# Kernel tuning notes

Measured on AMD Instinct MI355X. Metric: run time of the kernel, lower is better.

## Reference

```python
import jax, jax.numpy as jnp
import numpy as np

N, CIN, T, HF, WF = 1, 64, 8, 96, 96
C = 256
H, W = HF // 4, WF // 4
K = 27  # 3 dilations (1,3,5) x 3x3 kernel taps

# kernel-tap offsets, ordered: dilation-major, then row-major 3x3 (matches cat order)
_OFFS = np.array([(oy * d, ox * d) for d in (1, 3, 5) for oy in (-1, 0, 1) for ox in (-1, 0, 1)], dtype=np.float32)


def setup_inputs() -> dict:
    key = jax.random.key(0)
    ks = jax.random.split(key, 6)
    return {
        "input": jax.random.normal(ks[0], (N, CIN, T, HF, WF), jnp.float32),
        "flow": 2.0 * jax.random.normal(ks[1], (N, 2, T, H, W), jnp.float32),
        "w_node": 0.02 * jax.random.normal(ks[2], (C, CIN, 4, 4), jnp.float32),  # Conv3d(64,256,(1,4,4)) with unit time-kernel squeezed
        "b_node": jnp.zeros((C,), jnp.float32),
        "w_up": 0.02 * jax.random.normal(ks[3], (C, 64, 4, 4), jnp.float32),  # ConvTranspose3d(256,64,(1,4,4)) weight [in,out,kh,kw]
        "b_up": jnp.zeros((64,), jnp.float32),
        "w_out": 0.05 * jax.random.normal(ks[4], (64, 64), jnp.float32),  # 1x1x1 Conv3d(64,64)
        "b_out": jnp.zeros((64,), jnp.float32),
        "B": T,
    }


def _deform_sample(node, flow):
    # Deformable neighbor sampling for all 3 dilations at once.
    # node [N,C,T,H,W], flow [N,2,T,H,W] (y,x offsets) -> neighbour [N,C,T,H,W,K]
    n, c, t, h, w = node.shape
    off = jnp.asarray(_OFFS)  # [K,2]
    yy = jnp.arange(h, dtype=node.dtype)[:, None]   # [H,1]
    xx = jnp.arange(w, dtype=node.dtype)[None, :]   # [1,W]
    # sampling positions [N,T,K,H,W]
    py = (yy + off[:, 0][:, None, None]) + flow[:, 0][:, :, None]
    px = (xx + off[:, 1][:, None, None]) + flow[:, 1][:, :, None]
    y0 = jnp.floor(py)
    x0 = jnp.floor(px)
    ty = py - y0
    tx = px - x0
    y0 = y0.astype(jnp.int32)
    x0 = x0.astype(jnp.int32)
    nf = node.transpose(0, 2, 1, 3, 4).reshape(n, t, c, h * w)  # [N,T,C,HW]

    def gather(yi, xi):
        valid = ((yi >= 0) & (yi < h) & (xi >= 0) & (xi < w)).astype(node.dtype)
        idx = jnp.clip(yi, 0, h - 1) * w + jnp.clip(xi, 0, w - 1)  # [N,T,K,H,W]
        idx = jnp.broadcast_to(idx.reshape(n, t, 1, K * h * w), (n, t, c, K * h * w))
        v = jnp.take_along_axis(nf, idx, axis=-1).reshape(n, t, c, K, h, w)
        return v * valid[:, :, None]  # zero-pad outside

    samp = (gather(y0, x0) * ((1 - ty) * (1 - tx))[:, :, None]
            + gather(y0, x0 + 1) * ((1 - ty) * tx)[:, :, None]
            + gather(y0 + 1, x0) * (ty * (1 - tx))[:, :, None]
            + gather(y0 + 1, x0 + 1) * (ty * tx)[:, :, None])  # [N,T,C,K,H,W]
    return samp.transpose(0, 2, 1, 4, 5, 3)  # [N,C,T,H,W,K]


def reference(input, flow, w_node, b_node, w_up, b_up, w_out, b_out, B):
    n, cin, t, hf, wf = input.shape
    h, w = hf // 4, wf // 4
    # layer_node: kernel==stride (1,4,4) conv == non-overlapping 4x4 patch projection
    xr = input.reshape(n, cin, t, h, 4, w, 4)
    node = jnp.einsum('ncthawb,ocab->nothw', xr, w_node) + b_node[None, :, None, None, None]  # [N,C,T,H,W]
    c = node.shape[1]

    neighbour = _deform_sample(node, flow)  # [N,C,T,H,W,27] == cat(dcn1,dcn2,dcn3)

    nhw = n * h * w
    node_b = node.transpose(0, 3, 4, 2, 1).reshape(nhw, t, c)                      # [NHW,B,C]
    nb_a = neighbour.transpose(0, 3, 4, 1, 2, 5).reshape(nhw, c, t * K)            # [NHW,C,B*27]
    A = node_b @ nb_a                                                              # [NHW,B,B*27]
    nb_b = neighbour.transpose(0, 3, 4, 2, 5, 1).reshape(nhw, t * K, c)            # [NHW,B*27,C]
    out = (1.0 / 216.0) * (A @ nb_b)                                               # [NHW,B,C]
    out = out.reshape(n, h, w, t, c).transpose(0, 4, 3, 1, 2)                      # [N,C,T,H,W]

    # layer_out: ConvTranspose (k==stride, pad 0) == per-pixel 4x4 block expansion, then 1x1x1 conv
    up = jnp.einsum('ncthw,coab->nothawb', out, w_up).reshape(n, 64, t, 4 * h, 4 * w)
    up = up + b_up[None, :, None, None, None]
    return jnp.einsum('ncthw,oc->nothw', up, w_out) + b_out[None, :, None, None, None]
```

## Files before the change

kernel.cpp:

```cpp
#include <hip/hip_runtime.h>


typedef unsigned short ushort_t;
typedef ushort_t ushort8 __attribute__((ext_vector_type(8)));
typedef __bf16 bf16x8 __attribute__((ext_vector_type(8)));
typedef __bf16 bf16x2 __attribute__((ext_vector_type(2)));
typedef float f32x4 __attribute__((ext_vector_type(4)));
typedef unsigned int uint4v __attribute__((ext_vector_type(4)));

#define NSTR 264
#define TSTR 34
#define ASTR 40

__device__ __forceinline__ ushort_t f2bf(float f) {
    __bf16 h = (__bf16)f;
    return __builtin_bit_cast(ushort_t, h);
}
__device__ __forceinline__ float blo(unsigned u) { return __uint_as_float(u << 16); }
__device__ __forceinline__ float bhi(unsigned u) { return __uint_as_float(u & 0xffff0000u); }
__device__ __forceinline__ unsigned pk2(float a, float b) {
    bf16x2 v = { (__bf16)a, (__bf16)b };
    return __builtin_bit_cast(unsigned, v);
}
__device__ __forceinline__ unsigned pk2h(__bf16 a, __bf16 b) {
    bf16x2 v = { a, b };
    return __builtin_bit_cast(unsigned, v);
}
__device__ __forceinline__ void gld_lds16(const void* g, void* l) {
    __builtin_amdgcn_global_load_lds(
        (const __attribute__((address_space(1))) unsigned*)g,
        (__attribute__((address_space(3))) unsigned*)l, 16, 0, 0);
}

__global__ __launch_bounds__(256) void k_prep(
    const float* __restrict__ w_node, const float* __restrict__ w_up,
    const float* __restrict__ w_out, const float* __restrict__ b_up,
    const float* __restrict__ b_out,
    ushort_t* __restrict__ w_node_perm, ushort_t* __restrict__ Wf_perm,
    float* __restrict__ bias_tot)
{
    __shared__ float wout_s[4096];
    int tid = threadIdx.x;
    for (int i = tid; i < 4096; i += 256) wout_s[i] = w_out[i];
    __syncthreads();
    int gid = blockIdx.x * 256 + tid;
    #pragma unroll
    for (int r = 0; r < 4; ++r) {
        int e = gid + r * 65536;
        {
            int k = e & 1023, n = e >> 10;
            w_node_perm[(((k >> 3) << 8) + n) * 8 + (k & 7)] = f2bf(w_node[n * 1024 + k]);
        }
        {
            int n = e & 1023, k = e >> 10;
            int o = n >> 4, ab = n & 15;
            const float* wo = wout_s + o * 64;
            const float* wu = w_up + (k << 10) + ab;
            float s = 0.f;
            #pragma unroll 8
            for (int c = 0; c < 64; ++c) s += wo[c] * wu[c << 4];
            Wf_perm[(((k >> 3) << 10) + n) * 8 + (k & 7)] = f2bf(s);
        }
    }
    if (blockIdx.x == 0 && tid < 64) {
        float s = b_out[tid];
        const float* wo = wout_s + tid * 64;
        #pragma unroll 8
        for (int c = 0; c < 64; ++c) s += wo[c] * b_up[c];
        bias_tot[tid] = s;
    }
}

template<int FINAL>
__global__ __launch_bounds__(256) void k_gemm(
    const float* __restrict__ input, const ushort_t* __restrict__ a_bf,
    const ushort_t* __restrict__ w_perm, const float* __restrict__ bias,
    ushort_t* __restrict__ node_bf, float* __restrict__ dout)
{
    constexpr int KS = FINAL ? 4 : 16;
    constexpr int N  = FINAL ? 1024 : 256;
    __shared__ __align__(16) ushort_t A_lds[2][2048];
    __shared__ __align__(16) ushort_t B_lds[2][8192];
    int tid  = threadIdx.x;
    int lane = tid & 63, wid = tid >> 6;
    int g = lane >> 4, r16 = lane & 15;
    int m0 = blockIdx.x * 32, n0 = blockIdx.y * 128;

    const float*   inpA = nullptr;
    const ushort_t* finA = nullptr;
    int ldsA_slot;
    if constexpr (!FINAL) {
        int mA = tid & 31, kcA = tid >> 5;
        int m = m0 + mA;
        int t = m / 576, hw = m % 576, hh = hw / 24, ww = hw % 24;
        inpA = input + (size_t)(kcA >> 1) * 73728 + t * 9216 + hh * 384 + ww * 4 + (kcA & 1) * 192;
        ldsA_slot = (kcA * 32 + mA) * 8;
    } else {
        int m = m0 + (tid >> 3), q = tid & 7;
        finA = a_bf + m * 256 + ((q ^ (m & 7)) * 8);
        ldsA_slot = tid * 8;
    }

    f32x4 acc[2][2];
    #pragma unroll
    for (int i = 0; i < 2; ++i)
        #pragma unroll
        for (int j = 0; j < 2; ++j) acc[i][j] = (f32x4){0.f, 0.f, 0.f, 0.f};

    float4 fa, fb;
    #pragma unroll
    for (int r = 0; r < 4; ++r) {
        int s = r * 256 + tid;
        gld_lds16(w_perm + (size_t)(((s >> 7) * N + n0 + (s & 127)) * 8), &B_lds[0][s * 8]);
    }
    if constexpr (FINAL) {
        gld_lds16(finA, &A_lds[0][ldsA_slot]);
    } else {
        fa = *(const float4*)(inpA);
        fb = *(const float4*)(inpA + 96);
        uint4v p;
        p.x = pk2(fa.x, fa.y); p.y = pk2(fa.z, fa.w);
        p.z = pk2(fb.x, fb.y); p.w = pk2(fb.z, fb.w);
        *(uint4v*)&A_lds[0][ldsA_slot] = p;
    }
    __syncthreads();

    for (int kb = 0; kb < KS; ++kb) {
        int cur = kb & 1, nxt = cur ^ 1;
        bool more = (kb + 1 < KS);
        if (more) {
            #pragma unroll
            for (int r = 0; r < 4; ++r) {
                int s = r * 256 + tid;
                gld_lds16(w_perm + (size_t)((((kb + 1) * 8 + (s >> 7)) * N + n0 + (s & 127)) * 8),
                          &B_lds[nxt][s * 8]);
            }
            if constexpr (FINAL) {
                gld_lds16(finA + (kb + 1) * 64, &A_lds[nxt][ldsA_slot]);
            } else {
                fa = *(const float4*)(inpA + (size_t)(kb + 1) * 294912);
                fb = *(const float4*)(inpA + (size_t)(kb + 1) * 294912 + 96);
            }
        }
        bf16x8 af[2][2], bfr[2][2];
        #pragma unroll
        for (int mi = 0; mi < 2; ++mi)
            #pragma unroll
            for (int ks = 0; ks < 2; ++ks) {
                int idx;
                if constexpr (!FINAL) idx = ((ks * 4 + g) * 32 + mi * 16 + r16) * 8;
                else                  idx = (mi * 16 + r16) * 64 + (((ks * 4 + g) ^ (r16 & 7)) * 8);
                af[mi][ks] = __builtin_bit_cast(bf16x8, *(const ushort8*)&A_lds[cur][idx]);
            }
        #pragma unroll
        for (int ni = 0; ni < 2; ++ni)
            #pragma unroll
            for (int ks = 0; ks < 2; ++ks) {
                int idx = ((ks * 4 + g) * 128 + wid * 32 + ni * 16 + r16) * 8;
                bfr[ni][ks] = __builtin_bit_cast(bf16x8, *(const ushort8*)&B_lds[cur][idx]);
            }
        #pragma unroll
        for (int mi = 0; mi < 2; ++mi)
            #pragma unroll
            for (int ni = 0; ni < 2; ++ni)
                #pragma unroll
                for (int ks = 0; ks < 2; ++ks)
                    acc[mi][ni] = __builtin_amdgcn_mfma_f32_16x16x32_bf16(
                        af[mi][ks], bfr[ni][ks], acc[mi][ni], 0, 0, 0);
        if constexpr (!FINAL) {
            if (more) {
                uint4v p;
                p.x = pk2(fa.x, fa.y); p.y = pk2(fa.z, fa.w);
                p.z = pk2(fb.x, fb.y); p.w = pk2(fb.z, fb.w);
                *(uint4v*)&A_lds[nxt][ldsA_slot] = p;
            }
        }
        __syncthreads();
    }

    if constexpr (!FINAL) {
        #pragma unroll
        for (int ni = 0; ni < 2; ++ni) {
            int n = n0 + wid * 32 + ni * 16 + r16;
            float bv = bias[n];
            #pragma unroll
            for (int mi = 0; mi < 2; ++mi)
                #pragma unroll
                for (int rr = 0; rr < 4; ++rr) {
                    int m = m0 + mi * 16 + 4 * g + rr;
                    node_bf[(size_t)m * 256 + n] = f2bf(acc[mi][ni][rr] + bv);
                }
        }
    } else {
        #pragma unroll
        for (int ni = 0; ni < 2; ++ni) {
            int n = n0 + wid * 32 + ni * 16 + r16;
            int o = n >> 4, aa = (n >> 2) & 3, bb = n & 3;
            float bv = bias[o];
            #pragma unroll
            for (int mi = 0; mi < 2; ++mi)
                #pragma unroll
                for (int rr = 0; rr < 4; ++rr) {
                    int m = m0 + mi * 16 + 4 * g + rr;
                    int t = m / 576, hw = m % 576, hh = hw / 24, ww = hw % 24;
                    dout[((size_t)(o * 8 + t) * 96 + hh * 4 + aa) * 96 + ww * 4 + bb]
                        = acc[mi][ni][rr] + bv;
                }
        }
    }
}

__global__ __launch_bounds__(256) void k_attn(
    const ushort_t* __restrict__ node_bf, const float* __restrict__ flow,
    ushort_t* __restrict__ out_bf)
{
    __shared__ __align__(16) int      bases[224 * 4];
    __shared__ __align__(16) float    wts[224 * 4];
    __shared__ __align__(16) ushort_t neigh[32 * NSTR];
    __shared__ __align__(16) ushort_t neighT[256 * TSTR];
    __shared__ __align__(16) ushort_t A_s[16 * ASTR];

    int tid  = threadIdx.x;
    int pos  = blockIdx.x;
    int h    = pos / 24, w = pos % 24;
    int lane = tid & 63, wid = tid >> 6;
    int g    = lane >> 4, r16 = lane & 15;

    if (tid < 224) {
        int j = tid;
        float w00 = 0, w01 = 0, w10 = 0, w11 = 0;
        int b00 = 0, b01 = 0, b10 = 0, b11 = 0;
        if (j < 216) {
            int tt = j / 27, kk = j - tt * 27;
            int d  = 2 * (kk / 9) + 1;
            int oy = (kk / 3) % 3 - 1, ox = kk % 3 - 1;
            float fy = flow[tt * 576 + pos];
            float fx = flow[4608 + tt * 576 + pos];
            float py = (float)(h + oy * d) + fy;
            float px = (float)(w + ox * d) + fx;
            float fy0 = floorf(py), fx0 = floorf(px);
            int y0 = (int)fy0, x0 = (int)fx0;
            float ty = py - fy0, tx = px - fx0;
            int y0c = min(max(y0, 0), 23), y1c = min(max(y0 + 1, 0), 23);
            int x0c = min(max(x0, 0), 23), x1c = min(max(x0 + 1, 0), 23);
            float vy0 = (y0 >= 0 && y0 < 24) ? 1.f : 0.f;
            float vy1 = (y0 >= -1 && y0 < 23) ? 1.f : 0.f;
            float vx0 = (x0 >= 0 && x0 < 24) ? 1.f : 0.f;
            float vx1 = (x0 >= -1 && x0 < 23) ? 1.f : 0.f;
            w00 = (1.f - ty) * (1.f - tx) * vy0 * vx0;
            w01 = (1.f - ty) * tx * vy0 * vx1;
            w10 = ty * (1.f - tx) * vy1 * vx0;
            w11 = ty * tx * vy1 * vx1;
            int base_t = tt * 576 * 256;
            b00 = base_t + (y0c * 24 + x0c) * 256;
            b01 = base_t + (y0c * 24 + x1c) * 256;
            b10 = base_t + (y1c * 24 + x0c) * 256;
            b11 = base_t + (y1c * 24 + x1c) * 256;
        }
        bases[j * 4 + 0] = b00; bases[j * 4 + 1] = b01;
        bases[j * 4 + 2] = b10; bases[j * 4 + 3] = b11;
        wts[j * 4 + 0] = w00; wts[j * 4 + 1] = w01;
        wts[j * 4 + 2] = w10; wts[j * 4 + 3] = w11;
    }
    for (int i = tid; i < 320; i += 256) ((unsigned*)A_s)[i] = 0;

    bf16x8 nbf[8];
    if (wid < 2) {
        int t = r16;
        const ushort_t* src = node_bf + ((size_t)(t & 7) * 576 + pos) * 256 + g * 8;
        ushort8 uz = {};
        #pragma unroll
        for (int s = 0; s < 8; ++s) {
            ushort8 uu = *(const ushort8*)(src + s * 32);
            nbf[s] = __builtin_bit_cast(bf16x8, (t < 8) ? uu : uz);
        }
    }

    f32x4 oacc[4];
    #pragma unroll
    for (int i = 0; i < 4; ++i) oacc[i] = (f32x4){0.f, 0.f, 0.f, 0.f};

    __syncthreads();

    const int jp = tid >> 4;
    const int cb = tid & 15;

    uint4v rg[2][8];
    #define PREFETCH(TILE) {                                                   \
        int jA_ = (TILE) * 32 + jp * 2;                                        \
        int4 bsA_ = *(const int4*)&bases[jA_ * 4];                             \
        int4 bsB_ = *(const int4*)&bases[jA_ * 4 + 4];                         \
        _Pragma("unroll")                                                      \
        for (int q_ = 0; q_ < 2; ++q_) {                                       \
            int c0_ = cb * 16 + q_ * 8;                                        \
            rg[q_][0] = *(const uint4v*)(node_bf + bsA_.x + c0_);              \
            rg[q_][1] = *(const uint4v*)(node_bf + bsA_.y + c0_);              \
            rg[q_][2] = *(const uint4v*)(node_bf + bsA_.z + c0_);              \
            rg[q_][3] = *(const uint4v*)(node_bf + bsA_.w + c0_);              \
            rg[q_][4] = *(const uint4v*)(node_bf + bsB_.x + c0_);              \
            rg[q_][5] = *(const uint4v*)(node_bf + bsB_.y + c0_);              \
            rg[q_][6] = *(const uint4v*)(node_bf + bsB_.z + c0_);              \
            rg[q_][7] = *(const uint4v*)(node_bf + bsB_.w + c0_);              \
        } }

    PREFETCH(0);

    for (int tile = 0; tile < 7; ++tile) {
        {
            int jA = tile * 32 + jp * 2;
            int jl = jp * 2;
            float4 wA = *(const float4*)&wts[jA * 4];
            float4 wB = *(const float4*)&wts[jA * 4 + 4];
            #pragma unroll
            for (int q = 0; q < 2; ++q) {
                int c0 = cb * 16 + q * 8;
                uint4v outA, outB;
                #pragma unroll
                for (int p = 0; p < 4; ++p) {
                    unsigned a0 = rg[q][0][p], a1 = rg[q][1][p], a2 = rg[q][2][p], a3 = rg[q][3][p];
                    unsigned b0 = rg[q][4][p], b1 = rg[q][5][p], b2 = rg[q][6][p], b3 = rg[q][7][p];
                    float aL = wA.x * blo(a0) + wA.y * blo(a1) + wA.z * blo(a2) + wA.w * blo(a3);
                    float aH = wA.x * bhi(a0) + wA.y * bhi(a1) + wA.z * bhi(a2) + wA.w * bhi(a3);
                    float bL = wB.x * blo(b0) + wB.y * blo(b1) + wB.z * blo(b2) + wB.w * blo(b3);
                    float bH = wB.x * bhi(b0) + wB.y * bhi(b1) + wB.z * bhi(b2) + wB.w * bhi(b3);
                    __bf16 cAL = (__bf16)aL, cAH = (__bf16)aH;
                    __bf16 cBL = (__bf16)bL, cBH = (__bf16)bH;
                    outA[p] = pk2h(cAL, cAH);
                    outB[p] = pk2h(cBL, cBH);
                    *(unsigned*)(neighT + (c0 + 2 * p) * TSTR + jl)     = pk2h(cAL, cBL);
                    *(unsigned*)(neighT + (c0 + 2 * p + 1) * TSTR + jl) = pk2h(cAH, cBH);
                }
                *(uint4v*)(neigh + jl * NSTR + c0)       = outA;
                *(uint4v*)(neigh + (jl + 1) * NSTR + c0) = outB;
            }
        }
        if (tile < 6) PREFETCH(tile + 1);
        __syncthreads();

        if (wid < 2) {
            f32x4 aacc = {0.f, 0.f, 0.f, 0.f};
            int jbase = wid * 16;
            #pragma unroll
            for (int s = 0; s < 8; ++s) {
                const ushort_t* bp = neigh + (jbase + r16) * NSTR + s * 32 + g * 8;
                bf16x8 bfrag = __builtin_bit_cast(bf16x8, *(const ushort8*)bp);
                aacc = __builtin_amdgcn_mfma_f32_16x16x32_bf16(nbf[s], bfrag, aacc, 0, 0, 0);
            }
            if (g < 2) {
                #pragma unroll
                for (int rr = 0; rr < 4; ++rr)
                    A_s[(4 * g + rr) * ASTR + jbase + r16] = f2bf(aacc[rr] * (1.f / 216.f));
            }
        }
        __syncthreads();

        {
            bf16x8 afrag = __builtin_bit_cast(bf16x8, *(const ushort8*)(A_s + r16 * ASTR + g * 8));
            #pragma unroll
            for (int i = 0; i < 4; ++i) {
                const ushort_t* tp = neighT + (wid * 64 + i * 16 + r16) * TSTR + g * 8;
                uint4v uv;
                uv.x = *(const unsigned*)(tp);
                uv.y = *(const unsigned*)(tp + 2);
                uv.z = *(const unsigned*)(tp + 4);
                uv.w = *(const unsigned*)(tp + 6);
                bf16x8 bfrag = __builtin_bit_cast(bf16x8, uv);
                oacc[i] = __builtin_amdgcn_mfma_f32_16x16x32_bf16(afrag, bfrag, oacc[i], 0, 0, 0);
            }
        }
        __syncthreads();
    }
    #undef PREFETCH

    if (g < 2) {
        #pragma unroll
        for (int i = 0; i < 4; ++i) {
            int c = wid * 64 + i * 16 + r16;
            #pragma unroll
            for (int rr = 0; rr < 4; ++rr) {
                int t = 4 * g + rr;
                out_bf[((size_t)t * 576 + pos) * 256 + c] = f2bf(oacc[i][rr]);
            }
        }
    }
}

extern "C" void kernel_launch(void* const* d_in, const int* in_sizes, int n_in,
                              void* d_out, int out_size, void* d_ws, size_t ws_size,
                              hipStream_t stream) {
    (void)in_sizes; (void)n_in; (void)out_size; (void)ws_size;
    const float* input  = (const float*)d_in[0];
    const float* flow   = (const float*)d_in[1];
    const float* w_node = (const float*)d_in[2];
    const float* b_node = (const float*)d_in[3];
    const float* w_up   = (const float*)d_in[4];
    const float* b_up   = (const float*)d_in[5];
    const float* w_out  = (const float*)d_in[6];
    const float* b_out  = (const float*)d_in[7];
    float* dout = (float*)d_out;

    char* wsb = (char*)d_ws;
    ushort_t* node_bf = (ushort_t*)wsb;
    ushort_t* out_bf  = (ushort_t*)(wsb + 2359296);
    ushort_t* w_np    = (ushort_t*)(wsb + 4718592);
    ushort_t* wf_p    = (ushort_t*)(wsb + 5242880);
    float*    bias_t  = (float*)(wsb + 5767168);

    k_prep<<<256, 256, 0, stream>>>(w_node, w_up, w_out, b_up, b_out, w_np, wf_p, bias_t);
    k_gemm<0><<<dim3(144, 2), 256, 0, stream>>>(input, nullptr, w_np, b_node, node_bf, nullptr);
    k_attn<<<576, 256, 0, stream>>>(node_bf, flow, out_bf);
    k_gemm<1><<<dim3(144, 8), 256, 0, stream>>>(nullptr, out_bf, wf_p, bias_t, nullptr, dout);
}
```

Baseline: 74.84 us.

## Double-buffer attention neighbor tiles and narrow node GEMM N-tile

The attention kernel now double-buffers the neighbour tiles in dynamic shared memory, so the gather/combine for the next tile runs alongside the MFMA work on the current tile. This removes one barrier per tile. The first GEMM's N tile shrinks from 128 to 64, which doubles its grid to raise occupancy on a small problem. The cost is more LDS per attention block (about 77KB), which may lower occupancy, and each GEMM block does less reuse of the A tile.

```diff
diff --git a/kernel.cpp b/kernel.cpp
--- a/kernel.cpp
+++ b/kernel.cpp
@@ -11,6 +11,15 @@
 #define NSTR 264
 #define TSTR 34
 #define ASTR 40
+
+#define OFF_NH0   0
+#define OFF_NH1   16896
+#define OFF_NT0   33792
+#define OFF_NT1   51200
+#define OFF_AS    68608
+#define OFF_BASES 69888
+#define OFF_WTS   73472
+#define ATTN_LDS  77056
 
 __device__ __forceinline__ ushort_t f2bf(float f) {
     __bf16 h = (__bf16)f;
@@ -79,12 +88,15 @@
 {
     constexpr int KS = FINAL ? 4 : 16;
     constexpr int N  = FINAL ? 1024 : 256;
+    constexpr int BN = FINAL ? 128 : 64;
+    constexpr int NI = FINAL ? 2 : 1;
+    constexpr int RB = BN / 32;
     __shared__ __align__(16) ushort_t A_lds[2][2048];
-    __shared__ __align__(16) ushort_t B_lds[2][8192];
+    __shared__ __align__(16) ushort_t B_lds[2][BN * 64];
     int tid  = threadIdx.x;
     int lane = tid & 63, wid = tid >> 6;
     int g = lane >> 4, r16 = lane & 15;
-    int m0 = blockIdx.x * 32, n0 = blockIdx.y * 128;
+    int m0 = blockIdx.x * 32, n0 = blockIdx.y * BN;
 
     const float*   inpA = nullptr;
     const ushort_t* finA = nullptr;
@@ -101,17 +113,18 @@
         ldsA_slot = tid * 8;
     }
 
-    f32x4 acc[2][2];
+    f32x4 acc[2][NI];
     #pragma unroll
     for (int i = 0; i < 2; ++i)
         #pragma unroll
-        for (int j = 0; j < 2; ++j) acc[i][j] = (f32x4){0.f, 0.f, 0.f, 0.f};
+        for (int j = 0; j < NI; ++j) acc[i][j] = (f32x4){0.f, 0.f, 0.f, 0.f};
 
     float4 fa, fb;
     #pragma unroll
-    for (int r = 0; r < 4; ++r) {
+    for (int r = 0; r < RB; ++r) {
         int s = r * 256 + tid;
-        gld_lds16(w_perm + (size_t)(((s >> 7) * N + n0 + (s & 127)) * 8), &B_lds[0][s * 8]);
+        int kc = s / BN, n = s % BN;
+        gld_lds16(w_perm + (size_t)((kc * N + n0 + n) * 8), &B_lds[0][s * 8]);
     }
     if constexpr (FINAL) {
         gld_lds16(finA, &A_lds[0][ldsA_slot]);
@@ -130,9 +143,10 @@
         bool more = (kb + 1 < KS);
         if (more) {
             #pragma unroll
-            for (int r = 0; r < 4; ++r) {
+            for (int r = 0; r < RB; ++r) {
                 int s = r * 256 + tid;
-                gld_lds16(w_perm + (size_t)((((kb + 1) * 8 + (s >> 7)) * N + n0 + (s & 127)) * 8),
+                int kc = s / BN, n = s % BN;
+                gld_lds16(w_perm + (size_t)((((kb + 1) * 8 + kc) * N + n0 + n) * 8),
                           &B_lds[nxt][s * 8]);
             }
             if constexpr (FINAL) {
@@ -142,7 +156,7 @@
                 fb = *(const float4*)(inpA + (size_t)(kb + 1) * 294912 + 96);
             }
         }
-        bf16x8 af[2][2], bfr[2][2];
+        bf16x8 af[2][2], bfr[NI][2];
         #pragma unroll
         for (int mi = 0; mi < 2; ++mi)
             #pragma unroll
@@ -153,16 +167,16 @@
                 af[mi][ks] = __builtin_bit_cast(bf16x8, *(const ushort8*)&A_lds[cur][idx]);
             }
         #pragma unroll
-        for (int ni = 0; ni < 2; ++ni)
+        for (int ni = 0; ni < NI; ++ni)
             #pragma unroll
             for (int ks = 0; ks < 2; ++ks) {
-                int idx = ((ks * 4 + g) * 128 + wid * 32 + ni * 16 + r16) * 8;
+                int idx = ((ks * 4 + g) * BN + wid * (BN / 4) + ni * 16 + r16) * 8;
                 bfr[ni][ks] = __builtin_bit_cast(bf16x8, *(const ushort8*)&B_lds[cur][idx]);
             }
         #pragma unroll
         for (int mi = 0; mi < 2; ++mi)
             #pragma unroll
-            for (int ni = 0; ni < 2; ++ni)
+            for (int ni = 0; ni < NI; ++ni)
                 #pragma unroll
                 for (int ks = 0; ks < 2; ++ks)
                     acc[mi][ni] = __builtin_amdgcn_mfma_f32_16x16x32_bf16(
@@ -179,21 +193,18 @@
     }
 
     if constexpr (!FINAL) {
-        #pragma unroll
-        for (int ni = 0; ni < 2; ++ni) {
-            int n = n0 + wid * 32 + ni * 16 + r16;
-            float bv = bias[n];
-            #pragma unroll
-            for (int mi = 0; mi < 2; ++mi)
-                #pragma unroll
-                for (int rr = 0; rr < 4; ++rr) {
-                    int m = m0 + mi * 16 + 4 * g + rr;
-                    node_bf[(size_t)m * 256 + n] = f2bf(acc[mi][ni][rr] + bv);
-                }
-        }
+        int n = n0 + wid * 16 + r16;
+        float bv = bias[n];
+        #pragma unroll
+        for (int mi = 0; mi < 2; ++mi)
+            #pragma unroll
+            for (int rr = 0; rr < 4; ++rr) {
+                int m = m0 + mi * 16 + 4 * g + rr;
+                node_bf[(size_t)m * 256 + n] = f2bf(acc[mi][0][rr] + bv);
+            }
     } else {
         #pragma unroll
-        for (int ni = 0; ni < 2; ++ni) {
+        for (int ni = 0; ni < NI; ++ni) {
             int n = n0 + wid * 32 + ni * 16 + r16;
             int o = n >> 4, aa = (n >> 2) & 3, bb = n & 3;
             float bv = bias[o];
@@ -214,11 +225,10 @@
     const ushort_t* __restrict__ node_bf, const float* __restrict__ flow,
     ushort_t* __restrict__ out_bf)
 {
-    __shared__ __align__(16) int      bases[224 * 4];
-    __shared__ __align__(16) float    wts[224 * 4];
-    __shared__ __align__(16) ushort_t neigh[32 * NSTR];
-    __shared__ __align__(16) ushort_t neighT[256 * TSTR];
-    __shared__ __align__(16) ushort_t A_s[16 * ASTR];
+    extern __shared__ char smem[];
+    ushort_t* A_s   = (ushort_t*)(smem + OFF_AS);
+    int*      bases = (int*)(smem + OFF_BASES);
+    float*    wts   = (float*)(smem + OFF_WTS);
 
     int tid  = threadIdx.x;
     int pos  = blockIdx.x;
@@ -284,65 +294,70 @@
 
     const int jp = tid >> 4;
     const int cb = tid & 15;
-
     uint4v rg[2][8];
-    #define PREFETCH(TILE) {                                                   \
-        int jA_ = (TILE) * 32 + jp * 2;                                        \
-        int4 bsA_ = *(const int4*)&bases[jA_ * 4];                             \
-        int4 bsB_ = *(const int4*)&bases[jA_ * 4 + 4];                         \
-        _Pragma("unroll")                                                      \
-        for (int q_ = 0; q_ < 2; ++q_) {                                       \
-            int c0_ = cb * 16 + q_ * 8;                                        \
-            rg[q_][0] = *(const uint4v*)(node_bf + bsA_.x + c0_);              \
-            rg[q_][1] = *(const uint4v*)(node_bf + bsA_.y + c0_);              \
-            rg[q_][2] = *(const uint4v*)(node_bf + bsA_.z + c0_);              \
-            rg[q_][3] = *(const uint4v*)(node_bf + bsA_.w + c0_);              \
-            rg[q_][4] = *(const uint4v*)(node_bf + bsB_.x + c0_);              \
-            rg[q_][5] = *(const uint4v*)(node_bf + bsB_.y + c0_);              \
-            rg[q_][6] = *(const uint4v*)(node_bf + bsB_.z + c0_);              \
-            rg[q_][7] = *(const uint4v*)(node_bf + bsB_.w + c0_);              \
-        } }
-
-    PREFETCH(0);
-
-    for (int tile = 0; tile < 7; ++tile) {
-        {
-            int jA = tile * 32 + jp * 2;
-            int jl = jp * 2;
-            float4 wA = *(const float4*)&wts[jA * 4];
-            float4 wB = *(const float4*)&wts[jA * 4 + 4];
-            #pragma unroll
-            for (int q = 0; q < 2; ++q) {
-                int c0 = cb * 16 + q * 8;
-                uint4v outA, outB;
-                #pragma unroll
-                for (int p = 0; p < 4; ++p) {
-                    unsigned a0 = rg[q][0][p], a1 = rg[q][1][p], a2 = rg[q][2][p], a3 = rg[q][3][p];
-                    unsigned b0 = rg[q][4][p], b1 = rg[q][5][p], b2 = rg[q][6][p], b3 = rg[q][7][p];
-                    float aL = wA.x * blo(a0) + wA.y * blo(a1) + wA.z * blo(a2) + wA.w * blo(a3);
-                    float aH = wA.x * bhi(a0) + wA.y * bhi(a1) + wA.z * bhi(a2) + wA.w * bhi(a3);
-                    float bL = wB.x * blo(b0) + wB.y * blo(b1) + wB.z * blo(b2) + wB.w * blo(b3);
-                    float bH = wB.x * bhi(b0) + wB.y * bhi(b1) + wB.z * bhi(b2) + wB.w * bhi(b3);
-                    __bf16 cAL = (__bf16)aL, cAH = (__bf16)aH;
-                    __bf16 cBL = (__bf16)bL, cBH = (__bf16)bH;
-                    outA[p] = pk2h(cAL, cAH);
-                    outB[p] = pk2h(cBL, cBH);
-                    *(unsigned*)(neighT + (c0 + 2 * p) * TSTR + jl)     = pk2h(cAL, cBL);
-                    *(unsigned*)(neighT + (c0 + 2 * p + 1) * TSTR + jl) = pk2h(cAH, cBH);
-                }
-                *(uint4v*)(neigh + jl * NSTR + c0)       = outA;
-                *(uint4v*)(neigh + (jl + 1) * NSTR + c0) = outB;
-            }
-        }
-        if (tile < 6) PREFETCH(tile + 1);
-        __syncthreads();
+
+    auto prefetch = [&](int TILE) {
+        int jA = TILE * 32 + jp * 2;
+        int4 bsA = *(const int4*)&bases[jA * 4];
+        int4 bsB = *(const int4*)&bases[jA * 4 + 4];
+        #pragma unroll
+        for (int q = 0; q < 2; ++q) {
+            int c0 = cb * 16 + q * 8;
+            rg[q][0] = *(const uint4v*)(node_bf + bsA.x + c0);
+            rg[q][1] = *(const uint4v*)(node_bf + bsA.y + c0);
+            rg[q][2] = *(const uint4v*)(node_bf + bsA.z + c0);
+            rg[q][3] = *(const uint4v*)(node_bf + bsA.w + c0);
+            rg[q][4] = *(const uint4v*)(node_bf + bsB.x + c0);
+            rg[q][5] = *(const uint4v*)(node_bf + bsB.y + c0);
+            rg[q][6] = *(const uint4v*)(node_bf + bsB.z + c0);
+            rg[q][7] = *(const uint4v*)(node_bf + bsB.w + c0);
+        }
+    };
+    auto combine = [&](int TILE, ushort_t* nh, ushort_t* nt) {
+        int jA = TILE * 32 + jp * 2;
+        int jl = jp * 2;
+        float4 wA = *(const float4*)&wts[jA * 4];
+        float4 wB = *(const float4*)&wts[jA * 4 + 4];
+        #pragma unroll
+        for (int q = 0; q < 2; ++q) {
+            int c0 = cb * 16 + q * 8;
+            uint4v outA, outB;
+            #pragma unroll
+            for (int p = 0; p < 4; ++p) {
+                unsigned a0 = rg[q][0][p], a1 = rg[q][1][p], a2 = rg[q][2][p], a3 = rg[q][3][p];
+                unsigned b0 = rg[q][4][p], b1 = rg[q][5][p], b2 = rg[q][6][p], b3 = rg[q][7][p];
+                float aL = wA.x * blo(a0) + wA.y * blo(a1) + wA.z * blo(a2) + wA.w * blo(a3);
+                float aH = wA.x * bhi(a0) + wA.y * bhi(a1) + wA.z * bhi(a2) + wA.w * bhi(a3);
+                float bL = wB.x * blo(b0) + wB.y * blo(b1) + wB.z * blo(b2) + wB.w * blo(b3);
+                float bH = wB.x * bhi(b0) + wB.y * bhi(b1) + wB.z * bhi(b2) + wB.w * bhi(b3);
+                __bf16 cAL = (__bf16)aL, cAH = (__bf16)aH;
+                __bf16 cBL = (__bf16)bL, cBH = (__bf16)bH;
+                outA[p] = pk2h(cAL, cAH);
+                outB[p] = pk2h(cBL, cBH);
+                *(unsigned*)(nt + (c0 + 2 * p) * TSTR + jl)     = pk2h(cAL, cBL);
+                *(unsigned*)(nt + (c0 + 2 * p + 1) * TSTR + jl) = pk2h(cAH, cBH);
+            }
+            *(uint4v*)(nh + jl * NSTR + c0)       = outA;
+            *(uint4v*)(nh + (jl + 1) * NSTR + c0) = outB;
+        }
+    };
+
+    prefetch(0);
+    combine(0, (ushort_t*)(smem + OFF_NH0), (ushort_t*)(smem + OFF_NT0));
+    prefetch(1);
+    __syncthreads();
+
+    for (int k = 0; k < 7; ++k) {
+        int cur = k & 1;
+        ushort_t* nh = (ushort_t*)(smem + (cur ? OFF_NH1 : OFF_NH0));
+        ushort_t* nt = (ushort_t*)(smem + (cur ? OFF_NT1 : OFF_NT0));
 
         if (wid < 2) {
             f32x4 aacc = {0.f, 0.f, 0.f, 0.f};
             int jbase = wid * 16;
             #pragma unroll
             for (int s = 0; s < 8; ++s) {
-                const ushort_t* bp = neigh + (jbase + r16) * NSTR + s * 32 + g * 8;
+                const ushort_t* bp = nh + (jbase + r16) * NSTR + s * 32 + g * 8;
                 bf16x8 bfrag = __builtin_bit_cast(bf16x8, *(const ushort8*)bp);
                 aacc = __builtin_amdgcn_mfma_f32_16x16x32_bf16(nbf[s], bfrag, aacc, 0, 0, 0);
             }
@@ -358,7 +373,7 @@
             bf16x8 afrag = __builtin_bit_cast(bf16x8, *(const ushort8*)(A_s + r16 * ASTR + g * 8));
             #pragma unroll
             for (int i = 0; i < 4; ++i) {
-                const ushort_t* tp = neighT + (wid * 64 + i * 16 + r16) * TSTR + g * 8;
+                const ushort_t* tp = nt + (wid * 64 + i * 16 + r16) * TSTR + g * 8;
                 uint4v uv;
                 uv.x = *(const unsigned*)(tp);
                 uv.y = *(const unsigned*)(tp + 2);
@@ -368,9 +383,14 @@
                 oacc[i] = __builtin_amdgcn_mfma_f32_16x16x32_bf16(afrag, bfrag, oacc[i], 0, 0, 0);
             }
         }
+        if (k < 6) {
+            ushort_t* nh2 = (ushort_t*)(smem + (cur ? OFF_NH0 : OFF_NH1));
+            ushort_t* nt2 = (ushort_t*)(smem + (cur ? OFF_NT0 : OFF_NT1));
+            combine(k + 1, nh2, nt2);
+            if (k <= 4) prefetch(k + 2);
+        }
         __syncthreads();
     }
-    #undef PREFETCH
 
     if (g < 2) {
         #pragma unroll
@@ -407,7 +427,9 @@
     float*    bias_t  = (float*)(wsb + 5767168);
 
     k_prep<<<256, 256, 0, stream>>>(w_node, w_up, w_out, b_up, b_out, w_np, wf_p, bias_t);
-    k_gemm<0><<<dim3(144, 2), 256, 0, stream>>>(input, nullptr, w_np, b_node, node_bf, nullptr);
-    k_attn<<<576, 256, 0, stream>>>(node_bf, flow, out_bf);
+    k_gemm<0><<<dim3(144, 4), 256, 0, stream>>>(input, nullptr, w_np, b_node, node_bf, nullptr);
+    hipFuncSetAttribute(reinterpret_cast<const void*>(k_attn),
+                        hipFuncAttributeMaxDynamicSharedMemorySize, ATTN_LDS);
+    k_attn<<<576, 256, ATTN_LDS, stream>>>(node_bf, flow, out_bf);
     k_gemm<1><<<dim3(144, 8), 256, 0, stream>>>(nullptr, out_bf, wf_p, bias_t, nullptr, dout);
 }
```

Result: no change. 75.32 us (+0.6%).
